# Optimization experiments

Hardware: AMD Instinct MI355X
Metric: run time of the kernel (lower is better)

## Reference

```python
import jax, jax.numpy as jnp
import numpy as np

N_NODES = 50000
N_EDGES = 800000
EMBED_DIM = 128
VOCAB = 30000
BATCH = 1024
CTX_LEN = 50
NUM_LAYERS = 2
BN_EPS = 1e-5


def setup_inputs() -> dict:
    key = jax.random.key(0)
    ks = jax.random.split(key, 20)
    D = EMBED_DIM
    edge_index = jax.random.randint(ks[0], (2, N_EDGES), 0, N_NODES)
    norm = jax.random.uniform(ks[1], (N_EDGES,), dtype=jnp.float32) * 0.2  # GCN deg^-1/2 * deg^-1/2 weights
    ctx_ids = jax.random.randint(ks[2], (BATCH, CTX_LEN), 0, VOCAB)
    miss_ids = jax.random.randint(ks[3], (BATCH,), 0, VOCAB)
    vocab_to_fg = jnp.where(
        jax.random.uniform(ks[4], (VOCAB,)) < 0.5,
        jax.random.randint(ks[5], (VOCAB,), 0, N_NODES),
        -1,
    )
    emb_table = jax.random.normal(ks[6], (VOCAB, D), dtype=jnp.float32) * 0.02
    emb_table = emb_table.at[0].set(0.0)  # padding_idx=0
    fg_emb = jax.random.normal(ks[7], (N_NODES, D), dtype=jnp.float32) * 0.02
    gc_w = jax.random.normal(ks[8], (NUM_LAYERS, D, D), dtype=jnp.float32) * 0.02
    bn_gamma = jnp.ones((NUM_LAYERS, D), dtype=jnp.float32)
    bn_beta = jnp.zeros((NUM_LAYERS, D), dtype=jnp.float32)
    attn_w = jax.random.normal(ks[9], (D,), dtype=jnp.float32) * 0.02
    attn_b = jnp.zeros((), dtype=jnp.float32)
    fusion_w = jax.random.normal(ks[10], (D, 2 * D), dtype=jnp.float32) * 0.02
    fusion_b = jnp.zeros((D,), dtype=jnp.float32)
    proj1_w = jax.random.normal(ks[11], (2 * D, 2 * D), dtype=jnp.float32) * 0.02
    proj1_b = jnp.zeros((2 * D,), dtype=jnp.float32)
    proj2_w = jax.random.normal(ks[12], (D, 2 * D), dtype=jnp.float32) * 0.02
    proj2_b = jnp.zeros((D,), dtype=jnp.float32)
    return dict(edge_index=edge_index, norm=norm, ctx_ids=ctx_ids, miss_ids=miss_ids,
                vocab_to_fg=vocab_to_fg, emb_table=emb_table, fg_emb=fg_emb, gc_w=gc_w,
                bn_gamma=bn_gamma, bn_beta=bn_beta, attn_w=attn_w, attn_b=attn_b,
                fusion_w=fusion_w, fusion_b=fusion_b, proj1_w=proj1_w, proj1_b=proj1_b,
                proj2_w=proj2_w, proj2_b=proj2_b)


def reference(edge_index, norm, ctx_ids, miss_ids, vocab_to_fg, emb_table, fg_emb,
              gc_w, bn_gamma, bn_beta, attn_w, attn_b, fusion_w, fusion_b,
              proj1_w, proj1_b, proj2_w, proj2_b):
    N, D = fg_emb.shape
    row, col = edge_index[0], edge_index[1]
    # --- GCN stack: h <- h + BN(ReLU(Linear(A @ h))) ---
    h = fg_emb
    for l in range(gc_w.shape[0]):
        # sparse adj matmul: out[i] = sum_{(i,j) in E} norm_e * h[j]
        agg = jax.ops.segment_sum(norm[:, None] * h[col], row, num_segments=N)  # [N, D]
        z = jax.nn.relu(agg @ gc_w[l].T)
        mu = jnp.mean(z, axis=0)
        var = jnp.var(z, axis=0)  # biased, matches BN train-mode normalization
        h2 = (z - mu) * jax.lax.rsqrt(var + BN_EPS) * bn_gamma[l] + bn_beta[l]
        h = h + h2  # dropout is identity in eval reference
    graph_embs = h
    # --- context attention pooling ---
    ctx = emb_table[ctx_ids]                      # [B, L, D]
    logits = jnp.einsum('bld,d->bl', ctx, attn_w) + attn_b
    w = jax.nn.softmax(logits, axis=1)
    ctx_emb = jnp.einsum('bl,bld->bd', w, ctx)    # [B, D]
    # --- missing-ingredient embedding: vocab emb fused with gathered graph emb ---
    base = emb_table[miss_ids]                    # [B, D]
    fg_ids = vocab_to_fg[miss_ids]
    mask = fg_ids >= 0
    gp = jnp.where(mask[:, None], graph_embs[jnp.clip(fg_ids, 0)], 0.0)
    miss_emb = jnp.concatenate([base, gp], axis=-1) @ fusion_w.T + fusion_b
    # --- projection MLP ---
    q = jnp.concatenate([ctx_emb, miss_emb], axis=-1)
    q = jax.nn.relu(q @ proj1_w.T + proj1_b)
    query = q @ proj2_w.T + proj2_b
    return query, graph_embs
```

## Files before the change

### kernel.cpp

```cpp
#include <hip/hip_runtime.h>

#define NN 50000
#define NE 800000
#define DIM 128
#define NB 1024
#define CTXL 50
#define BN_EPS 1e-5f
#define STRIPS 3125
#define GEMM_BX 196
#define NBK 49
#define BCAP 20000
#define ABLK 1024
#define NAB 782

static const size_t OFF_Z    = 0;
static const size_t OFF_AH   = 6400000;
static const size_t OFF_HBF  = 9600000;
static const size_t OFF_EDG  = 12800000;
static const size_t OFF_RS   = 14400000;
static const size_t OFF_CUR  = 14450048;
static const size_t OFF_CNT  = 14500096;
static const size_t OFF_SCSH = 14550400;
static const size_t OFF_WH   = 14550656;
static const size_t OFF_WL   = 14567040;
static const size_t OFF_P2   = OFF_CUR;
static const size_t OFF_BKT  = OFF_Z + 3200000;
static const size_t OFF_ACNT = OFF_AH;
static const size_t OFF_AOFS = OFF_AH + 40000;
static const size_t OFF_BTOT = OFF_AH + 80000;
static const size_t OFF_QIN  = OFF_Z;
static const size_t OFF_CAT  = OFF_Z + 131072;
static const size_t OFF_Q1   = OFF_Z + 262144;
static const size_t OFF_FWB  = OFF_Z + 393216;
static const size_t OFF_P1B  = OFF_Z + 409600;
static const size_t OFF_P2B  = OFF_Z + 442368;

typedef __attribute__((ext_vector_type(8))) short s16x8;
typedef __attribute__((ext_vector_type(4))) float fx4;

__device__ __forceinline__ unsigned short f2bf(float f) {
    unsigned u = __float_as_uint(f);
    unsigned r = u + 0x7FFFu + ((u >> 16) & 1u);
    return (unsigned short)(r >> 16);
}
__device__ __forceinline__ float bf2f(unsigned short b) {
    return __uint_as_float((unsigned)b << 16);
}

__global__ __launch_bounds__(256) void binA_count(const int* __restrict__ row,
                                                  int* __restrict__ cnt) {
    __shared__ int c[NBK];
    int t = threadIdx.x;
    if (t < NBK) c[t] = 0;
    __syncthreads();
    int base = blockIdx.x * ABLK;
    #pragma unroll
    for (int k = 0; k < 4; k++) {
        int e = base + k * 256 + t;
        if (e < NE) atomicAdd(&c[row[e] >> 10], 1);
    }
    __syncthreads();
    if (t < NBK) cnt[t * 784 + blockIdx.x] = c[t];
}

__global__ __launch_bounds__(1024) void binA_scan(const int* __restrict__ cnt,
                                                  int* __restrict__ ofs,
                                                  int* __restrict__ btot) {
    __shared__ int lds[1024];
    int b = blockIdx.x, t = threadIdx.x;
    int v = (t < NAB) ? cnt[b * 784 + t] : 0;
    lds[t] = v;
    __syncthreads();
    for (int off = 1; off < 1024; off <<= 1) {
        int add = (t >= off) ? lds[t - off] : 0;
        __syncthreads();
        lds[t] += add;
        __syncthreads();
    }
    if (t < NAB) ofs[b * 784 + t] = lds[t] - v;
    if (t == NAB - 1) btot[b] = lds[t];
}

__global__ __launch_bounds__(256) void binA_scatter(const int* __restrict__ row,
                                                    const int* __restrict__ col,
                                                    const float* __restrict__ norm,
                                                    const int* __restrict__ ofs,
                                                    unsigned long long* __restrict__ bkt) {
    __shared__ int c[NBK], bofs[NBK], brsv[NBK];
    __shared__ unsigned long long stage[ABLK];
    __shared__ unsigned char stgb[ABLK];
    int t = threadIdx.x;
    if (t < NBK) c[t] = 0;
    __syncthreads();
    int base = blockIdx.x * ABLK;
    int my_b[4], my_i[4];
    unsigned long long my_pk[4];
    #pragma unroll
    for (int k = 0; k < 4; k++) {
        int e = base + k * 256 + t;
        if (e < NE) {
            int r = row[e];
            int b = r >> 10;
            my_b[k] = b;
            my_i[k] = atomicAdd(&c[b], 1);
            my_pk[k] = ((unsigned long long)__float_as_uint(norm[e]) << 32)
                     | ((unsigned long long)(unsigned)col[e] << 10)
                     | (unsigned)(r & 1023);
        } else my_b[k] = -1;
    }
    __syncthreads();
    if (t == 0) {
        int s = 0;
        for (int b = 0; b < NBK; b++) { bofs[b] = s; s += c[b]; }
    }
    if (t < NBK) brsv[t] = ofs[t * 784 + blockIdx.x];
    __syncthreads();
    #pragma unroll
    for (int k = 0; k < 4; k++) {
        if (my_b[k] >= 0) {
            int j = bofs[my_b[k]] + my_i[k];
            stage[j] = my_pk[k];
            stgb[j] = (unsigned char)my_b[k];
        }
    }
    __syncthreads();
    int tot = min(NE - base, ABLK);
    for (int j = t; j < tot; j += 256) {
        int b = stgb[j];
        int dst = brsv[b] + (j - bofs[b]);
        if (dst < BCAP) bkt[(size_t)b * BCAP + dst] = stage[j];
    }
}

__global__ __launch_bounds__(1024) void binB_rowstart(const unsigned long long* __restrict__ bkt,
                                                      const int* __restrict__ btot,
                                                      int* __restrict__ row_start) {
    __shared__ int c[1024];
    __shared__ int gofs_s;
    int b = blockIdx.x, t = threadIdx.x;
    c[t] = 0;
    if (t < 64) {
        int v = (t < b) ? btot[t] : 0;
        #pragma unroll
        for (int off = 32; off; off >>= 1) v += __shfl_down(v, off);
        if (t == 0) gofs_s = v;
    }
    __syncthreads();
    int n = btot[b];
    for (int i = t; i < n; i += 1024) {
        atomicAdd(&c[(int)(bkt[(size_t)b * BCAP + i] & 1023u)], 1);
    }
    __syncthreads();
    int myc = c[t];
    for (int off = 1; off < 1024; off <<= 1) {
        int add = (t >= off) ? c[t - off] : 0;
        __syncthreads();
        c[t] += add;
        __syncthreads();
    }
    int excl = gofs_s + c[t] - myc;
    int r = (b << 10) + t;
    if (r <= NN) row_start[r] = excl;
}

__global__ __launch_bounds__(1024) void binB_scatter(const unsigned long long* __restrict__ bkt,
                                                     const int* __restrict__ btot,
                                                     const int* __restrict__ row_start,
                                                     unsigned long long* __restrict__ edge_out) {
    __shared__ int cur[1024];
    int b = blockIdx.x, t = threadIdx.x;
    cur[t] = 0;
    __syncthreads();
    int n = btot[b];
    int rbase = b << 10;
    for (int i = t; i < n; i += 1024) {
        unsigned long long pk = bkt[(size_t)b * BCAP + i];
        int lr = (int)(pk & 1023u);
        unsigned colv = (unsigned)((pk >> 10) & 0xFFFFu);
        unsigned nrm = (unsigned)(pk >> 32);
        int k = atomicAdd(&cur[lr], 1);
        int pos = row_start[rbase + lr] + k;
        edge_out[pos] = ((unsigned long long)nrm << 32) | colv;
    }
}

__global__ void prep_kernel(const float* __restrict__ W, const float* __restrict__ fg,
                            unsigned short* __restrict__ Wh, unsigned short* __restrict__ Wl,
                            unsigned short* __restrict__ hbf) {
    int i = blockIdx.x * 256 + threadIdx.x;
    if (i < 2 * DIM * DIM) {
        float v = W[i];
        unsigned short h = f2bf(v);
        Wh[i] = h;
        Wl[i] = f2bf(v - bf2f(h));
    }
    if (i < NN * DIM / 4) {
        float4 v = reinterpret_cast<const float4*>(fg)[i];
        reinterpret_cast<ushort4*>(hbf)[i] =
            make_ushort4(f2bf(v.x), f2bf(v.y), f2bf(v.z), f2bf(v.w));
    }
}

__global__ __launch_bounds__(256) void agg_bf_kernel(const unsigned short* __restrict__ hbf,
                                                     const int* __restrict__ row_start,
                                                     const float* __restrict__ edge_s,
                                                     unsigned short* __restrict__ Ah) {
    int gw = (blockIdx.x * 256 + threadIdx.x) >> 6;
    int lane = threadIdx.x & 63;
    int half = lane >> 5;
    int c4 = (lane & 31) * 4;
    if (gw >= NN) return;
    int s = row_start[gw];
    int e = row_start[gw + 1];
    const int2* ep = (const int2*)edge_s;
    float a0 = 0.f, a1 = 0.f, a2 = 0.f, a3 = 0.f;
    int j = s + half;
    for (; j + 6 < e; j += 8) {
        int2 p0 = ep[j], p1 = ep[j + 2], p2 = ep[j + 4], p3 = ep[j + 6];
        ushort4 v0 = *(const ushort4*)(hbf + (size_t)p0.x * DIM + c4);
        ushort4 v1 = *(const ushort4*)(hbf + (size_t)p1.x * DIM + c4);
        ushort4 v2 = *(const ushort4*)(hbf + (size_t)p2.x * DIM + c4);
        ushort4 v3 = *(const ushort4*)(hbf + (size_t)p3.x * DIM + c4);
        float w0 = __int_as_float(p0.y), w1 = __int_as_float(p1.y);
        float w2 = __int_as_float(p2.y), w3 = __int_as_float(p3.y);
        a0 = fmaf(w0, bf2f(v0.x), a0); a1 = fmaf(w0, bf2f(v0.y), a1);
        a2 = fmaf(w0, bf2f(v0.z), a2); a3 = fmaf(w0, bf2f(v0.w), a3);
        a0 = fmaf(w1, bf2f(v1.x), a0); a1 = fmaf(w1, bf2f(v1.y), a1);
        a2 = fmaf(w1, bf2f(v1.z), a2); a3 = fmaf(w1, bf2f(v1.w), a3);
        a0 = fmaf(w2, bf2f(v2.x), a0); a1 = fmaf(w2, bf2f(v2.y), a1);
        a2 = fmaf(w2, bf2f(v2.z), a2); a3 = fmaf(w2, bf2f(v2.w), a3);
        a0 = fmaf(w3, bf2f(v3.x), a0); a1 = fmaf(w3, bf2f(v3.y), a1);
        a2 = fmaf(w3, bf2f(v3.z), a2); a3 = fmaf(w3, bf2f(v3.w), a3);
    }
    for (; j < e; j += 2) {
        int2 p = ep[j];
        ushort4 v = *(const ushort4*)(hbf + (size_t)p.x * DIM + c4);
        float w = __int_as_float(p.y);
        a0 = fmaf(w, bf2f(v.x), a0); a1 = fmaf(w, bf2f(v.y), a1);
        a2 = fmaf(w, bf2f(v.z), a2); a3 = fmaf(w, bf2f(v.w), a3);
    }
    a0 += __shfl_xor(a0, 32); a1 += __shfl_xor(a1, 32);
    a2 += __shfl_xor(a2, 32); a3 += __shfl_xor(a3, 32);
    if (half == 0) {
        *(ushort4*)(Ah + (size_t)gw * DIM + c4) =
            make_ushort4(f2bf(a0), f2bf(a1), f2bf(a2), f2bf(a3));
    }
}

__global__ __launch_bounds__(256) void gemm_mfma_kernel(const unsigned short* __restrict__ Ah,
                                                        const unsigned short* __restrict__ Wh,
                                                        const unsigned short* __restrict__ Wl,
                                                        unsigned short* __restrict__ zb,
                                                        float* __restrict__ P2) {
    __shared__ __align__(16) short Wlds[2][32][128];
    __shared__ float Pred[2][4][32];
    int tid = threadIdx.x;
    int lane = tid & 63;
    int w = tid >> 6;
    int r16 = lane & 15;
    int kg = lane >> 4;
    int cq = blockIdx.y;

    #pragma unroll
    for (int ff = 0; ff < 4; ff++) {
        int f = ff * 256 + tid;
        int plane = f >> 9;
        int c = (f >> 4) & 31;
        int ck = f & 15;
        const unsigned short* srcp = (plane ? Wl : Wh) + (size_t)(cq * 32 + c) * DIM + ck * 8;
        s16x8 v = *(const s16x8*)srcp;
        *(s16x8*)&Wlds[plane][c][(ck ^ (c & 7)) * 8] = v;
    }
    __syncthreads();

    int wv = (blockIdx.x * 256 + tid) >> 6;
    int nw = gridDim.x * 4;
    float bsum[2][4] = {{0.f}}, bsq[2][4] = {{0.f}};

    for (int strip = wv; strip < STRIPS; strip += nw) {
        size_t abase = (size_t)(strip * 16 + r16) * DIM + kg * 8;
        s16x8 b[4];
        #pragma unroll
        for (int ks = 0; ks < 4; ks++) b[ks] = *(const s16x8*)(Ah + abase + ks * 32);

        fx4 acc[2];
        acc[0] = (fx4){0.f, 0.f, 0.f, 0.f};
        acc[1] = (fx4){0.f, 0.f, 0.f, 0.f};
        #pragma unroll
        for (int ks = 0; ks < 4; ks++) {
            #pragma unroll
            for (int ct = 0; ct < 2; ct++) {
                int wrow = ct * 16 + r16;
                int wch = ((ks * 4 + kg) ^ (r16 & 7)) * 8;
                s16x8 wh8 = *(const s16x8*)&Wlds[0][wrow][wch];
                s16x8 wl8 = *(const s16x8*)&Wlds[1][wrow][wch];
                acc[ct] = __builtin_amdgcn_mfma_f32_16x16x32_bf16(wh8, b[ks], acc[ct], 0, 0, 0);
                acc[ct] = __builtin_amdgcn_mfma_f32_16x16x32_bf16(wl8, b[ks], acc[ct], 0, 0, 0);
            }
        }
        size_t zrow = (size_t)(strip * 16 + r16) * DIM + cq * 32 + kg * 4;
        #pragma unroll
        for (int ct = 0; ct < 2; ct++) {
            float x0 = fmaxf(acc[ct][0], 0.f);
            float x1 = fmaxf(acc[ct][1], 0.f);
            float x2 = fmaxf(acc[ct][2], 0.f);
            float x3 = fmaxf(acc[ct][3], 0.f);
            bsum[ct][0] += x0; bsq[ct][0] += x0 * x0;
            bsum[ct][1] += x1; bsq[ct][1] += x1 * x1;
            bsum[ct][2] += x2; bsq[ct][2] += x2 * x2;
            bsum[ct][3] += x3; bsq[ct][3] += x3 * x3;
            *(ushort4*)(zb + zrow + ct * 16) = make_ushort4(f2bf(x0), f2bf(x1), f2bf(x2), f2bf(x3));
        }
    }

    #pragma unroll
    for (int ct = 0; ct < 2; ct++) {
        #pragma unroll
        for (int jj = 0; jj < 4; jj++) {
            float s = bsum[ct][jj], q = bsq[ct][jj];
            #pragma unroll
            for (int off = 1; off <= 8; off <<= 1) {
                s += __shfl_xor(s, off);
                q += __shfl_xor(q, off);
            }
            if (r16 == 0) {
                int cpr = ct * 16 + kg * 4 + jj;
                Pred[0][w][cpr] = s;
                Pred[1][w][cpr] = q;
            }
        }
    }
    __syncthreads();
    if (tid < 64) {
        int kind = tid >> 5, cpr = tid & 31;
        float v = (Pred[kind][0][cpr] + Pred[kind][1][cpr]) +
                  (Pred[kind][2][cpr] + Pred[kind][3][cpr]);
        P2[blockIdx.x * 256 + cq * 64 + tid] = v;
    }
}

__global__ __launch_bounds__(256) void bn_finalize_kernel(const float* __restrict__ P2,
                                                          const float* __restrict__ gamma,
                                                          const float* __restrict__ beta,
                                                          float* __restrict__ scsh) {
    __shared__ float tot[256];
    int t = threadIdx.x;
    float a0 = 0.f, a1 = 0.f, a2 = 0.f, a3 = 0.f;
    for (int bx = 0; bx < GEMM_BX; bx += 4) {
        a0 += P2[(bx + 0) * 256 + t];
        a1 += P2[(bx + 1) * 256 + t];
        a2 += P2[(bx + 2) * 256 + t];
        a3 += P2[(bx + 3) * 256 + t];
    }
    tot[t] = (a0 + a1) + (a2 + a3);
    __syncthreads();
    if (t < 128) {
        int cq = t >> 5, cp = t & 31;
        float sum = tot[cq * 64 + cp];
        float sq  = tot[cq * 64 + 32 + cp];
        float mu = sum * (1.f / (float)NN);
        float var = sq * (1.f / (float)NN) - mu * mu;
        float sc = gamma[t] / sqrtf(var + BN_EPS);
        scsh[t] = sc;
        scsh[128 + t] = beta[t] - mu * sc;
    }
}

__global__ __launch_bounds__(256) void residual_kernel(const float* hin,
                                                       const unsigned short* zb,
                                                       const float* __restrict__ scsh,
                                                       float* hout,
                                                       unsigned short* hbf_out) {
    int i = blockIdx.x * 256 + threadIdx.x;
    if (i >= NN * DIM / 4) return;
    int c = (i * 4) & 127;
    ushort4 z4 = reinterpret_cast<const ushort4*>(zb)[i];
    float4 hv = reinterpret_cast<const float4*>(hin)[i];
    float4 sc = *reinterpret_cast<const float4*>(scsh + c);
    float4 sh = *reinterpret_cast<const float4*>(scsh + 128 + c);
    float4 o;
    o.x = hv.x + bf2f(z4.x) * sc.x + sh.x;
    o.y = hv.y + bf2f(z4.y) * sc.y + sh.y;
    o.z = hv.z + bf2f(z4.z) * sc.z + sh.z;
    o.w = hv.w + bf2f(z4.w) * sc.w + sh.w;
    reinterpret_cast<float4*>(hout)[i] = o;
    if (hbf_out) {
        ushort4 ob = make_ushort4(f2bf(o.x), f2bf(o.y), f2bf(o.z), f2bf(o.w));
        reinterpret_cast<ushort4*>(hbf_out)[i] = ob;
    }
}

__global__ __launch_bounds__(256) void pool_kernel(const int* __restrict__ ctx_ids,
                                                   const int* __restrict__ miss_ids,
                                                   const int* __restrict__ vocab_to_fg,
                                                   const float* __restrict__ emb_table,
                                                   const float* __restrict__ graph,
                                                   const float* __restrict__ attn_w,
                                                   const float* __restrict__ attn_b,
                                                   const float* __restrict__ fusion_w,
                                                   const float* __restrict__ proj1_w,
                                                   const float* __restrict__ proj2_w,
                                                   unsigned short* __restrict__ qinb,
                                                   unsigned short* __restrict__ catb,
                                                   unsigned short* __restrict__ fwb,
                                                   unsigned short* __restrict__ p1b,
                                                   unsigned short* __restrict__ p2b) {
    int b = blockIdx.x;
    int tid = threadIdx.x;
    __shared__ float ctx[CTXL][129];
    __shared__ float aw[128];
    __shared__ float lg[64];

    if (tid < 128) {
        int i = b * 128 + tid;
        if (i < 32768) fwb[i] = f2bf(fusion_w[i]);
        else if (i < 98304) p1b[i - 32768] = f2bf(proj1_w[i - 32768]);
        else p2b[i - 98304] = f2bf(proj2_w[i - 98304]);
    }

    if (tid < 128) aw[tid] = attn_w[tid];
    for (int f = tid; f < CTXL * 32; f += 256) {
        int t = f >> 5, d4 = (f & 31) * 4;
        int vid = ctx_ids[b * CTXL + t];
        float4 v = *(const float4*)(emb_table + (size_t)vid * DIM + d4);
        ctx[t][d4 + 0] = v.x; ctx[t][d4 + 1] = v.y;
        ctx[t][d4 + 2] = v.z; ctx[t][d4 + 3] = v.w;
    }
    __syncthreads();

    if (tid < CTXL) {
        float s = 0.f;
        for (int k = 0; k < 128; k++) s += ctx[tid][k] * aw[k];
        lg[tid] = s + attn_b[0];
    }
    __syncthreads();

    if (tid < 64) {
        float v = (tid < CTXL) ? lg[tid] : -INFINITY;
        float m = v;
        for (int off = 32; off; off >>= 1) m = fmaxf(m, __shfl_xor(m, off));
        float e = (tid < CTXL) ? expf(v - m) : 0.f;
        float s = e;
        for (int off = 32; off; off >>= 1) s += __shfl_xor(s, off);
        if (tid < CTXL) lg[tid] = e / s;
    }
    __syncthreads();

    int mid = miss_ids[b];
    if (tid < 128) {
        float s = 0.f;
        for (int t = 0; t < CTXL; t++) s += lg[t] * ctx[t][tid];
        qinb[(size_t)b * 256 + tid] = f2bf(s);
        catb[(size_t)b * 256 + tid] = f2bf(emb_table[(size_t)mid * DIM + tid]);
    } else {
        int d = tid - 128;
        int fg = vocab_to_fg[mid];
        float gp = (fg >= 0) ? graph[(size_t)fg * DIM + d] : 0.f;
        catb[(size_t)b * 256 + tid] = f2bf(gp);
    }
}

__global__ __launch_bounds__(256) void head_gemm_kernel(const unsigned short* __restrict__ A,
                                                        const unsigned short* __restrict__ W,
                                                        const float* __restrict__ bias,
                                                        unsigned short* __restrict__ outb,
                                                        float* __restrict__ outf,
                                                        int ocol, int ostride, int relu) {
    __shared__ __align__(16) short Wlds[64][256];
    int tid = threadIdx.x;
    int lane = tid & 63;
    int r16 = lane & 15;
    int kg = lane >> 4;
    int cgb = blockIdx.y * 64;

    #pragma unroll
    for (int ff = 0; ff < 8; ff++) {
        int f = ff * 256 + tid;
        int c = f >> 5;
        int ck = f & 31;
        s16x8 v = *(const s16x8*)(W + (size_t)(cgb + c) * 256 + ck * 8);
        *(s16x8*)&Wlds[c][(ck ^ (c & 7)) * 8] = v;
    }
    __syncthreads();

    int w = tid >> 6;
    int row = blockIdx.x * 16 + r16;

    size_t abase = (size_t)row * 256 + kg * 8;
    s16x8 bfrag[8];
    #pragma unroll
    for (int ks = 0; ks < 8; ks++) bfrag[ks] = *(const s16x8*)(A + abase + ks * 32);

    fx4 acc = (fx4){0.f, 0.f, 0.f, 0.f};
    int wrow = w * 16 + r16;
    #pragma unroll
    for (int ks = 0; ks < 8; ks++) {
        int wch = (((ks * 4 + kg) ^ (r16 & 7))) * 8;
        s16x8 w8 = *(const s16x8*)&Wlds[wrow][wch];
        acc = __builtin_amdgcn_mfma_f32_16x16x32_bf16(w8, bfrag[ks], acc, 0, 0, 0);
    }

    int cbase = cgb + w * 16 + kg * 4;
    float4 o;
    o.x = acc[0] + bias[cbase + 0];
    o.y = acc[1] + bias[cbase + 1];
    o.z = acc[2] + bias[cbase + 2];
    o.w = acc[3] + bias[cbase + 3];
    if (relu) {
        o.x = fmaxf(o.x, 0.f); o.y = fmaxf(o.y, 0.f);
        o.z = fmaxf(o.z, 0.f); o.w = fmaxf(o.w, 0.f);
    }
    size_t op = (size_t)row * ostride + ocol + cbase;
    if (outb) {
        *(ushort4*)(outb + op) = make_ushort4(f2bf(o.x), f2bf(o.y), f2bf(o.z), f2bf(o.w));
    } else {
        *(float4*)(outf + op) = o;
    }
}

extern "C" void kernel_launch(void* const* d_in, const int* in_sizes, int n_in,
                              void* d_out, int out_size, void* d_ws, size_t ws_size,
                              hipStream_t stream) {
    const int*   edge_index = (const int*)d_in[0];
    const float* norm       = (const float*)d_in[1];
    const int*   ctx_ids    = (const int*)d_in[2];
    const int*   miss_ids   = (const int*)d_in[3];
    const int*   vocab_to_fg= (const int*)d_in[4];
    const float* emb_table  = (const float*)d_in[5];
    const float* fg_emb     = (const float*)d_in[6];
    const float* gc_w       = (const float*)d_in[7];
    const float* bn_gamma   = (const float*)d_in[8];
    const float* bn_beta    = (const float*)d_in[9];
    const float* attn_w     = (const float*)d_in[10];
    const float* attn_b     = (const float*)d_in[11];
    const float* fusion_w   = (const float*)d_in[12];
    const float* fusion_b   = (const float*)d_in[13];
    const float* proj1_w    = (const float*)d_in[14];
    const float* proj1_b    = (const float*)d_in[15];
    const float* proj2_w    = (const float*)d_in[16];
    const float* proj2_b    = (const float*)d_in[17];

    const int* row = edge_index;
    const int* col = edge_index + NE;

    float* ws = (float*)d_ws;
    unsigned short* zb     = (unsigned short*)(ws + OFF_Z);
    unsigned short* Ah     = (unsigned short*)(ws + OFF_AH);
    unsigned short* hbf    = (unsigned short*)(ws + OFF_HBF);
    float*          edge_s = ws + OFF_EDG;
    int*   row_start = (int*)(ws + OFF_RS);
    float* scsh      = ws + OFF_SCSH;
    unsigned short* Wh = (unsigned short*)(ws + OFF_WH);
    unsigned short* Wl = (unsigned short*)(ws + OFF_WL);
    float* P2        = ws + OFF_P2;
    unsigned long long* bkt = (unsigned long long*)(ws + OFF_BKT);
    int*   acnt      = (int*)(ws + OFF_ACNT);
    int*   aofs      = (int*)(ws + OFF_AOFS);
    int*   btot      = (int*)(ws + OFF_BTOT);
    unsigned short* qinb = (unsigned short*)(ws + OFF_QIN);
    unsigned short* catb = (unsigned short*)(ws + OFF_CAT);
    unsigned short* q1b  = (unsigned short*)(ws + OFF_Q1);
    unsigned short* fwb  = (unsigned short*)(ws + OFF_FWB);
    unsigned short* p1b  = (unsigned short*)(ws + OFF_P1B);
    unsigned short* p2b  = (unsigned short*)(ws + OFF_P2B);

    float* query = (float*)d_out;
    float* G     = (float*)d_out + (size_t)NB * DIM;

    binA_count<<<NAB, 256, 0, stream>>>(row, acnt);
    binA_scan<<<NBK, 1024, 0, stream>>>(acnt, aofs, btot);
    binA_scatter<<<NAB, 256, 0, stream>>>(row, col, norm, aofs, bkt);
    binB_rowstart<<<NBK, 1024, 0, stream>>>(bkt, btot, row_start);
    binB_scatter<<<NBK, 1024, 0, stream>>>(bkt, btot, row_start, (unsigned long long*)edge_s);

    prep_kernel<<<6250, 256, 0, stream>>>(gc_w, fg_emb, Wh, Wl, hbf);

    const int AGG_B = NN / 4;
    const int RES_B = (NN * DIM / 4) / 256;
    dim3 gemm_grid(GEMM_BX, 4);

    agg_bf_kernel<<<AGG_B, 256, 0, stream>>>(hbf, row_start, edge_s, Ah);
    gemm_mfma_kernel<<<gemm_grid, 256, 0, stream>>>(Ah, Wh, Wl, zb, P2);
    bn_finalize_kernel<<<1, 256, 0, stream>>>(P2, bn_gamma, bn_beta, scsh);
    residual_kernel<<<RES_B, 256, 0, stream>>>(fg_emb, zb, scsh, G, hbf);

    agg_bf_kernel<<<AGG_B, 256, 0, stream>>>(hbf, row_start, edge_s, Ah);
    gemm_mfma_kernel<<<gemm_grid, 256, 0, stream>>>(Ah, Wh + DIM * DIM, Wl + DIM * DIM, zb, P2);
    bn_finalize_kernel<<<1, 256, 0, stream>>>(P2, bn_gamma + 128, bn_beta + 128, scsh);
    residual_kernel<<<RES_B, 256, 0, stream>>>(G, zb, scsh, G, nullptr);

    pool_kernel<<<NB, 256, 0, stream>>>(ctx_ids, miss_ids, vocab_to_fg, emb_table, G,
                                        attn_w, attn_b, fusion_w, proj1_w, proj2_w,
                                        qinb, catb, fwb, p1b, p2b);
    dim3 hg2(64, 2), hg4(64, 4);
    head_gemm_kernel<<<hg2, 256, 0, stream>>>(catb, fwb, fusion_b, qinb, nullptr, 128, 256, 0);
    head_gemm_kernel<<<hg4, 256, 0, stream>>>(qinb, p1b, proj1_b, q1b, nullptr, 0, 256, 1);
    head_gemm_kernel<<<hg2, 256, 0, stream>>>(q1b, p2b, proj2_b, nullptr, query, 0, 128, 0);
}
```

Before: 201.1 us.

## Fuse CSR build kernels and restructure GEMM to full-width column tiles per block

Merges the bucket-count pass with the weight/feature bf16 prep kernel, and merges the row-start and scatter passes of the CSR build into one kernel that keeps row starts in LDS. This cuts two launches and one global round-trip of row_start. The GEMM now loads the whole 128x128 hi/lo weight into LDS. Each block covers all output columns of its 16-row strip, with one wave per 32-column slice, over 512 blocks instead of a 196x4 grid. Each wave writes its BN partial sums straight to global memory. The block-level LDS reduction is gone, and bn_finalize reduces the partials with 1024 threads. The trade-off is 64KB of LDS per GEMM block, which limits occupancy, and P2 now shares workspace with the bucket buffer.

```diff
diff --git a/kernel.cpp b/kernel.cpp
--- a/kernel.cpp
+++ b/kernel.cpp
@@ -7,7 +7,7 @@
 #define CTXL 50
 #define BN_EPS 1e-5f
 #define STRIPS 3125
-#define GEMM_BX 196
+#define GEMM_BLOCKS 512
 #define NBK 49
 #define BCAP 20000
 #define ABLK 1024
@@ -18,13 +18,11 @@
 static const size_t OFF_HBF  = 9600000;
 static const size_t OFF_EDG  = 12800000;
 static const size_t OFF_RS   = 14400000;
-static const size_t OFF_CUR  = 14450048;
-static const size_t OFF_CNT  = 14500096;
 static const size_t OFF_SCSH = 14550400;
 static const size_t OFF_WH   = 14550656;
 static const size_t OFF_WL   = 14567040;
-static const size_t OFF_P2   = OFF_CUR;
 static const size_t OFF_BKT  = OFF_Z + 3200000;
+static const size_t OFF_P2   = OFF_Z + 3200000;
 static const size_t OFF_ACNT = OFF_AH;
 static const size_t OFF_AOFS = OFF_AH + 40000;
 static const size_t OFF_BTOT = OFF_AH + 80000;
@@ -47,20 +45,39 @@
     return __uint_as_float((unsigned)b << 16);
 }
 
-__global__ __launch_bounds__(256) void binA_count(const int* __restrict__ row,
-                                                  int* __restrict__ cnt) {
-    __shared__ int c[NBK];
-    int t = threadIdx.x;
-    if (t < NBK) c[t] = 0;
-    __syncthreads();
-    int base = blockIdx.x * ABLK;
-    #pragma unroll
-    for (int k = 0; k < 4; k++) {
-        int e = base + k * 256 + t;
-        if (e < NE) atomicAdd(&c[row[e] >> 10], 1);
-    }
-    __syncthreads();
-    if (t < NBK) cnt[t * 784 + blockIdx.x] = c[t];
+__global__ __launch_bounds__(256) void csr_prep_kernel(const int* __restrict__ row,
+                                                       const float* __restrict__ W,
+                                                       const float* __restrict__ fg,
+                                                       int* __restrict__ cnt,
+                                                       unsigned short* __restrict__ Wh,
+                                                       unsigned short* __restrict__ Wl,
+                                                       unsigned short* __restrict__ hbf) {
+    int i = blockIdx.x * 256 + threadIdx.x;
+    if (i < 2 * DIM * DIM) {
+        float v = W[i];
+        unsigned short h = f2bf(v);
+        Wh[i] = h;
+        Wl[i] = f2bf(v - bf2f(h));
+    }
+    if (i < NN * DIM / 4) {
+        float4 v = reinterpret_cast<const float4*>(fg)[i];
+        reinterpret_cast<ushort4*>(hbf)[i] =
+            make_ushort4(f2bf(v.x), f2bf(v.y), f2bf(v.z), f2bf(v.w));
+    }
+    if (blockIdx.x < NAB) {
+        __shared__ int c[NBK];
+        int t = threadIdx.x;
+        if (t < NBK) c[t] = 0;
+        __syncthreads();
+        int base = blockIdx.x * ABLK;
+        #pragma unroll
+        for (int k = 0; k < 4; k++) {
+            int e = base + k * 256 + t;
+            if (e < NE) atomicAdd(&c[row[e] >> 10], 1);
+        }
+        __syncthreads();
+        if (t < NBK) cnt[t * 784 + blockIdx.x] = c[t];
+    }
 }
 
 __global__ __launch_bounds__(1024) void binA_scan(const int* __restrict__ cnt,
@@ -132,10 +149,12 @@
     }
 }
 
-__global__ __launch_bounds__(1024) void binB_rowstart(const unsigned long long* __restrict__ bkt,
-                                                      const int* __restrict__ btot,
-                                                      int* __restrict__ row_start) {
+__global__ __launch_bounds__(1024) void binB_kernel(const unsigned long long* __restrict__ bkt,
+                                                    const int* __restrict__ btot,
+                                                    int* __restrict__ row_start,
+                                                    unsigned long long* __restrict__ edge_out) {
     __shared__ int c[1024];
+    __shared__ int rs[1024];
     __shared__ int gofs_s;
     int b = blockIdx.x, t = threadIdx.x;
     c[t] = 0;
@@ -147,9 +166,9 @@
     }
     __syncthreads();
     int n = btot[b];
-    for (int i = t; i < n; i += 1024) {
-        atomicAdd(&c[(int)(bkt[(size_t)b * BCAP + i] & 1023u)], 1);
-    }
+    size_t bb = (size_t)b * BCAP;
+    for (int i = t; i < n; i += 1024)
+        atomicAdd(&c[(int)(bkt[bb + i] & 1023u)], 1);
     __syncthreads();
     int myc = c[t];
     for (int off = 1; off < 1024; off <<= 1) {
@@ -159,45 +178,19 @@
         __syncthreads();
     }
     int excl = gofs_s + c[t] - myc;
+    rs[t] = excl;
     int r = (b << 10) + t;
     if (r <= NN) row_start[r] = excl;
-}
-
-__global__ __launch_bounds__(1024) void binB_scatter(const unsigned long long* __restrict__ bkt,
-                                                     const int* __restrict__ btot,
-                                                     const int* __restrict__ row_start,
-                                                     unsigned long long* __restrict__ edge_out) {
-    __shared__ int cur[1024];
-    int b = blockIdx.x, t = threadIdx.x;
-    cur[t] = 0;
-    __syncthreads();
-    int n = btot[b];
-    int rbase = b << 10;
+    __syncthreads();
+    c[t] = 0;
+    __syncthreads();
     for (int i = t; i < n; i += 1024) {
-        unsigned long long pk = bkt[(size_t)b * BCAP + i];
+        unsigned long long pk = bkt[bb + i];
         int lr = (int)(pk & 1023u);
         unsigned colv = (unsigned)((pk >> 10) & 0xFFFFu);
         unsigned nrm = (unsigned)(pk >> 32);
-        int k = atomicAdd(&cur[lr], 1);
-        int pos = row_start[rbase + lr] + k;
-        edge_out[pos] = ((unsigned long long)nrm << 32) | colv;
-    }
-}
-
-__global__ void prep_kernel(const float* __restrict__ W, const float* __restrict__ fg,
-                            unsigned short* __restrict__ Wh, unsigned short* __restrict__ Wl,
-                            unsigned short* __restrict__ hbf) {
-    int i = blockIdx.x * 256 + threadIdx.x;
-    if (i < 2 * DIM * DIM) {
-        float v = W[i];
-        unsigned short h = f2bf(v);
-        Wh[i] = h;
-        Wl[i] = f2bf(v - bf2f(h));
-    }
-    if (i < NN * DIM / 4) {
-        float4 v = reinterpret_cast<const float4*>(fg)[i];
-        reinterpret_cast<ushort4*>(hbf)[i] =
-            make_ushort4(f2bf(v.x), f2bf(v.y), f2bf(v.z), f2bf(v.w));
+        int k = atomicAdd(&c[lr], 1);
+        edge_out[rs[lr] + k] = ((unsigned long long)nrm << 32) | colv;
     }
 }
 
@@ -252,32 +245,27 @@
                                                         const unsigned short* __restrict__ Wl,
                                                         unsigned short* __restrict__ zb,
                                                         float* __restrict__ P2) {
-    __shared__ __align__(16) short Wlds[2][32][128];
-    __shared__ float Pred[2][4][32];
+    __shared__ __align__(16) short Wlds[2][128][128];
     int tid = threadIdx.x;
     int lane = tid & 63;
     int w = tid >> 6;
     int r16 = lane & 15;
     int kg = lane >> 4;
-    int cq = blockIdx.y;
-
-    #pragma unroll
-    for (int ff = 0; ff < 4; ff++) {
+
+    #pragma unroll
+    for (int ff = 0; ff < 16; ff++) {
         int f = ff * 256 + tid;
-        int plane = f >> 9;
-        int c = (f >> 4) & 31;
+        int plane = f >> 11;
+        int c = (f >> 4) & 127;
         int ck = f & 15;
-        const unsigned short* srcp = (plane ? Wl : Wh) + (size_t)(cq * 32 + c) * DIM + ck * 8;
-        s16x8 v = *(const s16x8*)srcp;
-        *(s16x8*)&Wlds[plane][c][(ck ^ (c & 7)) * 8] = v;
-    }
-    __syncthreads();
-
-    int wv = (blockIdx.x * 256 + tid) >> 6;
-    int nw = gridDim.x * 4;
+        const unsigned short* srcp = (plane ? Wl : Wh) + (size_t)c * DIM + ck * 8;
+        *(s16x8*)&Wlds[plane][c][(ck ^ (c & 7)) * 8] = *(const s16x8*)srcp;
+    }
+    __syncthreads();
+
     float bsum[2][4] = {{0.f}}, bsq[2][4] = {{0.f}};
 
-    for (int strip = wv; strip < STRIPS; strip += nw) {
+    for (int strip = blockIdx.x; strip < STRIPS; strip += GEMM_BLOCKS) {
         size_t abase = (size_t)(strip * 16 + r16) * DIM + kg * 8;
         s16x8 b[4];
         #pragma unroll
@@ -290,7 +278,7 @@
         for (int ks = 0; ks < 4; ks++) {
             #pragma unroll
             for (int ct = 0; ct < 2; ct++) {
-                int wrow = ct * 16 + r16;
+                int wrow = w * 32 + ct * 16 + r16;
                 int wch = ((ks * 4 + kg) ^ (r16 & 7)) * 8;
                 s16x8 wh8 = *(const s16x8*)&Wlds[0][wrow][wch];
                 s16x8 wl8 = *(const s16x8*)&Wlds[1][wrow][wch];
@@ -298,7 +286,7 @@
                 acc[ct] = __builtin_amdgcn_mfma_f32_16x16x32_bf16(wl8, b[ks], acc[ct], 0, 0, 0);
             }
         }
-        size_t zrow = (size_t)(strip * 16 + r16) * DIM + cq * 32 + kg * 4;
+        size_t zrow = (size_t)(strip * 16 + r16) * DIM + w * 32 + kg * 4;
         #pragma unroll
         for (int ct = 0; ct < 2; ct++) {
             float x0 = fmaxf(acc[ct][0], 0.f);
@@ -324,45 +312,40 @@
                 q += __shfl_xor(q, off);
             }
             if (r16 == 0) {
-                int cpr = ct * 16 + kg * 4 + jj;
-                Pred[0][w][cpr] = s;
-                Pred[1][w][cpr] = q;
+                int ch = w * 32 + ct * 16 + kg * 4 + jj;
+                P2[blockIdx.x * 256 + ch] = s;
+                P2[blockIdx.x * 256 + 128 + ch] = q;
             }
         }
     }
-    __syncthreads();
-    if (tid < 64) {
-        int kind = tid >> 5, cpr = tid & 31;
-        float v = (Pred[kind][0][cpr] + Pred[kind][1][cpr]) +
-                  (Pred[kind][2][cpr] + Pred[kind][3][cpr]);
-        P2[blockIdx.x * 256 + cq * 64 + tid] = v;
-    }
-}
-
-__global__ __launch_bounds__(256) void bn_finalize_kernel(const float* __restrict__ P2,
-                                                          const float* __restrict__ gamma,
-                                                          const float* __restrict__ beta,
-                                                          float* __restrict__ scsh) {
-    __shared__ float tot[256];
-    int t = threadIdx.x;
+}
+
+__global__ __launch_bounds__(1024) void bn_finalize_kernel(const float* __restrict__ P2,
+                                                           const float* __restrict__ gamma,
+                                                           const float* __restrict__ beta,
+                                                           float* __restrict__ scsh) {
+    __shared__ float tot[4][256];
+    int t = threadIdx.x & 255;
+    int g = threadIdx.x >> 8;
     float a0 = 0.f, a1 = 0.f, a2 = 0.f, a3 = 0.f;
-    for (int bx = 0; bx < GEMM_BX; bx += 4) {
-        a0 += P2[(bx + 0) * 256 + t];
-        a1 += P2[(bx + 1) * 256 + t];
-        a2 += P2[(bx + 2) * 256 + t];
-        a3 += P2[(bx + 3) * 256 + t];
-    }
-    tot[t] = (a0 + a1) + (a2 + a3);
-    __syncthreads();
-    if (t < 128) {
-        int cq = t >> 5, cp = t & 31;
-        float sum = tot[cq * 64 + cp];
-        float sq  = tot[cq * 64 + 32 + cp];
+    int base = g * (GEMM_BLOCKS / 4);
+    for (int bx = 0; bx < GEMM_BLOCKS / 4; bx += 4) {
+        a0 += P2[(size_t)(base + bx + 0) * 256 + t];
+        a1 += P2[(size_t)(base + bx + 1) * 256 + t];
+        a2 += P2[(size_t)(base + bx + 2) * 256 + t];
+        a3 += P2[(size_t)(base + bx + 3) * 256 + t];
+    }
+    tot[g][t] = (a0 + a1) + (a2 + a3);
+    __syncthreads();
+    if (threadIdx.x < 128) {
+        int c = threadIdx.x;
+        float sum = (tot[0][c] + tot[1][c]) + (tot[2][c] + tot[3][c]);
+        float sq  = (tot[0][128 + c] + tot[1][128 + c]) + (tot[2][128 + c] + tot[3][128 + c]);
         float mu = sum * (1.f / (float)NN);
         float var = sq * (1.f / (float)NN) - mu * mu;
-        float sc = gamma[t] / sqrtf(var + BN_EPS);
-        scsh[t] = sc;
-        scsh[128 + t] = beta[t] - mu * sc;
+        float sc = gamma[c] / sqrtf(var + BN_EPS);
+        scsh[c] = sc;
+        scsh[128 + c] = beta[c] - mu * sc;
     }
 }
 
@@ -567,26 +550,22 @@
     float* query = (float*)d_out;
     float* G     = (float*)d_out + (size_t)NB * DIM;
 
-    binA_count<<<NAB, 256, 0, stream>>>(row, acnt);
+    csr_prep_kernel<<<6250, 256, 0, stream>>>(row, gc_w, fg_emb, acnt, Wh, Wl, hbf);
     binA_scan<<<NBK, 1024, 0, stream>>>(acnt, aofs, btot);
     binA_scatter<<<NAB, 256, 0, stream>>>(row, col, norm, aofs, bkt);
-    binB_rowstart<<<NBK, 1024, 0, stream>>>(bkt, btot, row_start);
-    binB_scatter<<<NBK, 1024, 0, stream>>>(bkt, btot, row_start, (unsigned long long*)edge_s);
-
-    prep_kernel<<<6250, 256, 0, stream>>>(gc_w, fg_emb, Wh, Wl, hbf);
+    binB_kernel<<<NBK, 1024, 0, stream>>>(bkt, btot, row_start, (unsigned long long*)edge_s);
 
     const int AGG_B = NN / 4;
     const int RES_B = (NN * DIM / 4) / 256;
-    dim3 gemm_grid(GEMM_BX, 4);
 
     agg_bf_kernel<<<AGG_B, 256, 0, stream>>>(hbf, row_start, edge_s, Ah);
-    gemm_mfma_kernel<<<gemm_grid, 256, 0, stream>>>(Ah, Wh, Wl, zb, P2);
-    bn_finalize_kernel<<<1, 256, 0, stream>>>(P2, bn_gamma, bn_beta, scsh);
+    gemm_mfma_kernel<<<GEMM_BLOCKS, 256, 0, stream>>>(Ah, Wh, Wl, zb, P2);
+    bn_finalize_kernel<<<1, 1024, 0, stream>>>(P2, bn_gamma, bn_beta, scsh);
     residual_kernel<<<RES_B, 256, 0, stream>>>(fg_emb, zb, scsh, G, hbf);
 
     agg_bf_kernel<<<AGG_B, 256, 0, stream>>>(hbf, row_start, edge_s, Ah);
-    gemm_mfma_kernel<<<gemm_grid, 256, 0, stream>>>(Ah, Wh + DIM * DIM, Wl + DIM * DIM, zb, P2);
-    bn_finalize_kernel<<<1, 256, 0, stream>>>(P2, bn_gamma + 128, bn_beta + 128, scsh);
+    gemm_mfma_kernel<<<GEMM_BLOCKS, 256, 0, stream>>>(Ah, Wh + DIM * DIM, Wl + DIM * DIM, zb, P2);
+    bn_finalize_kernel<<<1, 1024, 0, stream>>>(P2, bn_gamma + 128, bn_beta + 128, scsh);
     residual_kernel<<<RES_B, 256, 0, stream>>>(G, zb, scsh, G, nullptr);
 
     pool_kernel<<<NB, 256, 0, stream>>>(ctx_ids, miss_ids, vocab_to_fg, emb_table, G,
```

After: 192.6 us. 4.2% less time.
